# Optimization experiments

Hardware: AMD Instinct MI355X
Metric: run time of the kernel (lower is better)

Reference implementation:

```python
import jax, jax.numpy as jnp
import numpy as np

GROUPS = 8
HEADS = 8
EPS = 1e-5


def group_norm(x, w, b, groups=GROUPS, eps=EPS):
    # x: [B, C, D, H, W]
    B, C, D, H, W = x.shape
    xg = x.reshape(B, groups, C // groups, D, H, W)
    mu = xg.mean(axis=(2, 3, 4, 5), keepdims=True)
    var = xg.var(axis=(2, 3, 4, 5), keepdims=True)
    xn = ((xg - mu) / jnp.sqrt(var + eps)).reshape(B, C, D, H, W)
    return xn * w[None, :, None, None, None] + b[None, :, None, None, None]


def conv1x1(x, w, b):
    # 1x1x1 Conv3d == channel-mixing GEMM. w: [Cout, Cin], x: [B, Cin, D, H, W]
    y = jnp.einsum('oc,bcdhw->bodhw', w, x)
    return y + b[None, :, None, None, None]


def setup_inputs() -> dict:
    key = jax.random.key(0)
    ks = jax.random.split(key, 8)
    C, CTX = 512, 512
    B, D, H, W = 1, 16, 16, 16
    x = jax.random.normal(ks[0], (B, C, D, H, W), dtype=jnp.float32)
    context = jax.random.normal(ks[1], (B, CTX, D, H, W), dtype=jnp.float32)
    return {
        'x': x,
        'context': context,
        'norm_w': jnp.ones((C,), jnp.float32),
        'norm_b': jnp.zeros((C,), jnp.float32),
        'normc_w': jnp.ones((CTX,), jnp.float32),
        'normc_b': jnp.zeros((CTX,), jnp.float32),
        'q_w': jax.random.normal(ks[2], (C, C), jnp.float32) * 0.02,
        'q_b': jnp.zeros((C,), jnp.float32),
        'kv_w': jax.random.normal(ks[3], (2 * C, CTX), jnp.float32) * 0.02,
        'kv_b': jnp.zeros((2 * C,), jnp.float32),
        'proj_w': jax.random.normal(ks[4], (C, C), jnp.float32) * 0.02,
        'proj_b': jnp.zeros((C,), jnp.float32),
    }


def _split_heads(t, heads):
    # [B, (h c), D, H, W] -> [B, h, S, c] with S = D*H*W
    B, C, D, H, W = t.shape
    return t.reshape(B, heads, C // heads, D * H * W).transpose(0, 1, 3, 2)


def reference(x, context, norm_w, norm_b, normc_w, normc_b,
              q_w, q_b, kv_w, kv_b, proj_w, proj_b):
    B, C, D, H, W = x.shape
    h = group_norm(x, norm_w, norm_b)
    c = group_norm(context, normc_w, normc_b)
    q = conv1x1(h, q_w, q_b)
    kv = conv1x1(c, kv_w, kv_b)
    k, v = jnp.split(kv, 2, axis=1)
    q = _split_heads(q, HEADS)   # [B, h, S, c]
    k = _split_heads(k, HEADS)
    v = _split_heads(v, HEADS)
    scale = (C // HEADS) ** (-0.5)
    logits = jnp.einsum('bhqc,bhkc->bhqk', q, k) * scale
    attn = jax.nn.softmax(logits, axis=-1)
    out = jnp.einsum('bhqk,bhkc->bhqc', attn, v)
    # [B, h, S, c] -> [B, (h c), D, H, W]
    out = out.transpose(0, 1, 3, 2).reshape(B, C, D, H, W)
    out = conv1x1(out, proj_w, proj_b)
    return x + out
```

## Files before the change

### kernel.cpp

```cpp
#include <hip/hip_runtime.h>

typedef unsigned short u16;
typedef unsigned int u32;
typedef float f32x4 __attribute__((ext_vector_type(4)));
typedef __bf16 bf16x8 __attribute__((ext_vector_type(8)));
typedef u32 u32x4 __attribute__((ext_vector_type(4)));
typedef u32 u32x2 __attribute__((ext_vector_type(2)));
typedef short s16x4 __attribute__((ext_vector_type(4)));

#define LOG2E 1.44269504088896340736f

static __device__ __forceinline__ u16 f2bf(float f){ u32 u=__builtin_bit_cast(u32,f); u32 r=u+0x7fffu+((u>>16)&1u); return (u16)(r>>16); }
static __device__ __forceinline__ u32 pk2(float a,float b){ return (u32)f2bf(a)|((u32)f2bf(b)<<16); }
static __device__ __forceinline__ float fexp2(float x){
#if __has_builtin(__builtin_amdgcn_exp2f)
  return __builtin_amdgcn_exp2f(x);
#else
  float r; asm volatile("v_exp_f32 %0, %1" : "=v"(r) : "v"(x)); return r;
#endif
}
static __device__ __forceinline__ f32x4 mfma16(u32x4 a,u32x4 b,f32x4 c){
  return __builtin_amdgcn_mfma_f32_16x16x32_bf16(__builtin_bit_cast(bf16x8,a),__builtin_bit_cast(bf16x8,b),c,0,0,0);
}
#if __has_builtin(__builtin_amdgcn_mfma_f32_16x16x16bf16_1k)
static __device__ __forceinline__ f32x4 mfma1k(s16x4 a,s16x4 b,f32x4 c){
  return __builtin_amdgcn_mfma_f32_16x16x16bf16_1k(a,b,c,0,0,0);
}
#else
static __device__ __forceinline__ f32x4 mfma1k(s16x4 a,s16x4 b,f32x4 c){
  f32x4 d; asm("v_mfma_f32_16x16x16_bf16 %0, %1, %2, %3":"=v"(d):"v"(a),"v"(b),"v"(c)); return d;
}
#endif
static __device__ __forceinline__ u32x4 ldfrag(const u32* p){
  uint2 a=*(const uint2*)p; uint2 b=*(const uint2*)(p+2);
  u32x4 r; r.x=a.x; r.y=a.y; r.z=b.x; r.w=b.y; return r;
}
static __device__ __forceinline__ s16x4 ld8(const u32* p){
  return __builtin_bit_cast(s16x4, *(const u32x2*)p);
}
static __device__ __forceinline__ void stlds(u32* d, uint4 v){
  *(uint2*)d = make_uint2(v.x,v.y); *(uint2*)(d+2) = make_uint2(v.z,v.w);
}
static __device__ __forceinline__ uint4 pack8(float4 a,float4 b){
  uint4 o; o.x=pk2(a.x,a.y); o.y=pk2(a.z,a.w); o.z=pk2(b.x,b.y); o.w=pk2(b.z,b.w); return o;
}

__global__ __launch_bounds__(256) void k_stats(const float* __restrict__ x, const float* __restrict__ c,
                                               float* __restrict__ stats){
  const int g=blockIdx.x>>3, slice=blockIdx.x&7;
  const float* src=(g<8?x:c)+(size_t)(g&7)*262144+(size_t)slice*32768;
  const float4* p=(const float4*)src;
  const int t=threadIdx.x;
  float s1=0.f,s2=0.f;
  for(int i=0;i<32;i++){
    float4 v=p[t+i*256];
    s1+=v.x+v.y+v.z+v.w;
    s2+=v.x*v.x+v.y*v.y+v.z*v.z+v.w*v.w;
  }
  #pragma unroll
  for(int m=1;m<64;m<<=1){ s1+=__shfl_xor(s1,m,64); s2+=__shfl_xor(s2,m,64); }
  __shared__ float r1[4],r2[4];
  const int lane=t&63,w=t>>6;
  if(lane==0){ r1[w]=s1; r2[w]=s2; }
  __syncthreads();
  if(t==0){
    atomicAdd(&stats[2*g],   r1[0]+r1[1]+r1[2]+r1[3]);
    atomicAdd(&stats[2*g+1], r2[0]+r2[1]+r2[2]+r2[3]);
  }
}

__global__ __launch_bounds__(256) void k_prep(const float* __restrict__ qw,const float* __restrict__ qb,
    const float* __restrict__ kvw,const float* __restrict__ kvb,
    const float* __restrict__ nw,const float* __restrict__ nb,
    const float* __restrict__ ncw,const float* __restrict__ ncb,
    const float* __restrict__ pb,const float* __restrict__ stats,
    u16* __restrict__ Wall,float* __restrict__ biasAll){
  const int lane=threadIdx.x&63, w=threadIdx.x>>6;
  const int r=blockIdx.x*4+w;
  if(r>=1536){ if(lane==0) biasAll[r]=pb[r-1536]; return; }
  const bool isq = r<512;
  const float* Wsrc = isq ? qw+(size_t)r*512 : kvw+(size_t)(r-512)*512;
  const float* anw = isq ? nw : ncw;
  const float* anb = isq ? nb : ncb;
  const int gbase = isq ? 0 : 8;
  const float bin = isq ? qb[r] : kvb[r-512];
  const int ci0=lane*8;
  float4 wa=*(const float4*)(Wsrc+ci0);
  float4 wb=*(const float4*)(Wsrc+ci0+4);
  float wf[8]={wa.x,wa.y,wa.z,wa.w,wb.x,wb.y,wb.z,wb.w};
  float bp=0.f; u16 hb[8];
  #pragma unroll
  for(int j=0;j<8;j++){
    int ci=ci0+j;
    int g=gbase+(ci>>6);
    float mean=stats[2*g]*(1.f/262144.f);
    float var =stats[2*g+1]*(1.f/262144.f)-mean*mean;
    float rstd=rsqrtf(var+1e-5f);
    float alv=anw[ci]*rstd;
    float bev=anb[ci]-mean*alv;
    bp+=wf[j]*bev;
    hb[j]=f2bf(wf[j]*alv);
  }
  uint4 ov;
  ov.x=(u32)hb[0]|((u32)hb[1]<<16);
  ov.y=(u32)hb[2]|((u32)hb[3]<<16);
  ov.z=(u32)hb[4]|((u32)hb[5]<<16);
  ov.w=(u32)hb[6]|((u32)hb[7]<<16);
  *(uint4*)(Wall+(size_t)r*512+ci0)=ov;
  #pragma unroll
  for(int m=1;m<64;m<<=1) bp+=__shfl_xor(bp,m,64);
  if(lane==0) biasAll[r]=bin+bp;
}

template<int AMODE,int BMODE,int SMODE,int ZM>
__global__ __launch_bounds__(256) void k_gemm(const void* __restrict__ Av,const void* __restrict__ Av2,
    const void* __restrict__ Bv,const float* __restrict__ biasAll,const float* __restrict__ residf,
    void* __restrict__ out1,void* __restrict__ out2,float scale1,float scale2){
  __shared__ __align__(16) u32 As[2][64*18];
  __shared__ __align__(16) u32 Bs[2][128*18];
  const int t=threadIdx.x, lane=t&63, w=t>>6;
  const int wm=w&1, wn=w>>1, quad=lane>>4, l15=lane&15;
  const int m0=blockIdx.y*64, n0=blockIdx.x*128;
  const int z = ZM ? blockIdx.z : 0;
  const void* Aptr = (ZM && z) ? Av2 : Av;
  const u16* Bu = (const u16*)Bv + (BMODE==0 ? (size_t)z*512*512 : 0);
  const float* Bf = (const float*)Bv;
  const float* bias = biasAll + (ZM ? z*512 : 0);
  void* outv = (ZM && z) ? out2 : out1;
  const float scale = (ZM && z) ? scale2 : scale1;
  const int arow=t>>2, akc=(t&3)*8;
  const int cl=t>>3, s8=(t&7)*8;

  uint4 ra; float4 raf0, raf1;
  uint4 rb0, rb1; float4 rbf0, rbf1, rbf2, rbf3;

  auto loadAB=[&](int kk){
    if(AMODE==0){
      const u16* A=(const u16*)Aptr;
      ra=*(const uint4*)(A+(size_t)(m0+arow)*512+kk+akc);
    }else if(AMODE==1){
      const float* A=(const float*)Aptr;
      raf0=*(const float4*)(A+(size_t)(kk+cl)*4096+m0+s8);
      raf1=*(const float4*)(A+(size_t)(kk+cl)*4096+m0+s8+4);
    }else{
      const float* A=(const float*)Aptr;
      raf0=*(const float4*)(A+(size_t)(m0+arow)*512+kk+akc);
      raf1=*(const float4*)(A+(size_t)(m0+arow)*512+kk+akc+4);
    }
    if(BMODE==2){
      rbf0=*(const float4*)(Bf+(size_t)(kk+cl)*4096+n0+s8);
      rbf1=*(const float4*)(Bf+(size_t)(kk+cl)*4096+n0+s8+4);
      rbf2=*(const float4*)(Bf+(size_t)(kk+cl)*4096+n0+64+s8);
      rbf3=*(const float4*)(Bf+(size_t)(kk+cl)*4096+n0+64+s8+4);
    }else if(BMODE==1){
      rb0=*(const uint4*)(Bu+((size_t)((kk>>6)*4096+n0+arow))*64+(kk&63)+akc);
      rb1=*(const uint4*)(Bu+((size_t)((kk>>6)*4096+n0+64+arow))*64+(kk&63)+akc);
    }else{
      rb0=*(const uint4*)(Bu+(size_t)(n0+arow)*512+kk+akc);
      rb1=*(const uint4*)(Bu+(size_t)(n0+64+arow)*512+kk+akc);
    }
  };
  auto writeAB=[&](u32* Asb,u32* Bsb){
    if(AMODE==0){ stlds(&Asb[arow*18+(akc>>1)],ra); }
    else if(AMODE==1){
      float f[8]={raf0.x,raf0.y,raf0.z,raf0.w,raf1.x,raf1.y,raf1.z,raf1.w};
      u16* As16=(u16*)Asb;
      #pragma unroll
      for(int j=0;j<8;j++) As16[(s8+j)*36+cl]=f2bf(f[j]);
    }else{
      stlds(&Asb[arow*18+(akc>>1)],pack8(raf0,raf1));
    }
    if(BMODE==2){
      u16* Bs16=(u16*)Bsb;
      float f[8]={rbf0.x,rbf0.y,rbf0.z,rbf0.w,rbf1.x,rbf1.y,rbf1.z,rbf1.w};
      float g[8]={rbf2.x,rbf2.y,rbf2.z,rbf2.w,rbf3.x,rbf3.y,rbf3.z,rbf3.w};
      #pragma unroll
      for(int j=0;j<8;j++){
        Bs16[(s8+j)*36+cl]=f2bf(f[j]);
        Bs16[(64+s8+j)*36+cl]=f2bf(g[j]);
      }
    }else{
      stlds(&Bsb[arow*18+(akc>>1)],rb0);
      stlds(&Bsb[(64+arow)*18+(akc>>1)],rb1);
    }
  };

  f32x4 acc[2][4];
  #pragma unroll
  for(int i=0;i<2;i++)
    #pragma unroll
    for(int j=0;j<4;j++){ acc[i][j].x=0.f; acc[i][j].y=0.f; acc[i][j].z=0.f; acc[i][j].w=0.f; }

  auto compute=[&](const u32* Asb,const u32* Bsb){
    const u32* Ab=Asb+(wm*32+l15)*18+quad*4;
    const u32* Bb=Bsb+(wn*64+l15)*18+quad*4;
    u32x4 af[2], bfr[4];
    #pragma unroll
    for(int mt=0;mt<2;mt++) af[mt]=ldfrag(Ab+mt*288);
    #pragma unroll
    for(int nt=0;nt<4;nt++) bfr[nt]=ldfrag(Bb+nt*288);
    #pragma unroll
    for(int mt=0;mt<2;mt++)
      #pragma unroll
      for(int nt=0;nt<4;nt++) acc[mt][nt]=mfma16(af[mt],bfr[nt],acc[mt][nt]);
  };

  loadAB(0); writeAB(As[0],Bs[0]);
  __syncthreads();
  for(int kk=0;kk<512;kk+=64){
    loadAB(kk+32);
    compute(As[0],Bs[0]);
    writeAB(As[1],Bs[1]);
    __syncthreads();
    const bool n2=(kk+64)<512;
    if(n2) loadAB(kk+64);
    compute(As[1],Bs[1]);
    if(n2){ writeAB(As[0],Bs[0]); __syncthreads(); }
  }
  #pragma unroll
  for(int mt=0;mt<2;mt++)
    #pragma unroll
    for(int nt=0;nt<4;nt++){
      const int n = n0 + wn*64 + nt*16 + l15;
      if(SMODE==0){
        u16* out=(u16*)outv;
        const float bn = bias[n];
        const size_t base = ((size_t)((n>>6)*4096))*64 + (size_t)(n&63);
        #pragma unroll
        for(int r=0;r<4;r++){
          int m = m0 + wm*32 + mt*16 + quad*4 + r;
          out[base + (size_t)m*64] = f2bf((acc[mt][nt][r]+bn)*scale);
        }
      } else if(SMODE==1){
        u16* out=(u16*)outv;
        #pragma unroll
        for(int r=0;r<4;r++){
          int m = m0 + wm*32 + mt*16 + quad*4 + r;
          out[(size_t)m*4096+n] = f2bf(acc[mt][nt][r] + bias[m]);
        }
      } else {
        float* out=(float*)outv;
        #pragma unroll
        for(int r=0;r<4;r++){
          int m = m0 + wm*32 + mt*16 + quad*4 + r;
          out[(size_t)m*4096+n] = acc[mt][nt][r] + bias[m] + residf[(size_t)m*4096+n];
        }
      }
    }
}

__global__ __launch_bounds__(512,4) void k_attn(const u16* __restrict__ Qh,const u16* __restrict__ Kh,
                                              const u16* __restrict__ Vp,u16* __restrict__ Oh){
  __shared__ __align__(16) u32 KS[2][2][64*34];
  __shared__ __align__(16) u32 VS[2][2][64*34];
  const int t=threadIdx.x, lane=t&63, w=t>>6, quad=lane>>4, l15=lane&15;
  const int half=w>>2, wq=w&3;
  const int h=blockIdx.y, s0=blockIdx.x*64;
  const int tt=t&255, srow=tt>>2, sc=(tt&3)*16;
  const u16* Kg = Kh + ((size_t)(h*4096 + half*2048 + srow))*64 + sc;
  const u16* Vg = Vp + (size_t)(h*64+srow)*4096 + half*2048 + sc;
  const u16* Qg = Qh + ((size_t)(h*4096+s0+wq*16+l15))*64;
  s16x4 qf[4];
  #pragma unroll
  for(int kc=0;kc<4;kc++) qf[kc]=ld8((const u32*)(Qg + kc*16 + quad*4));

  uint4 pk0,pk1,pv0,pv1;
  auto loadKV=[&](int t0l){
    const u16* kp=Kg+(size_t)t0l*64;
    pk0=*(const uint4*)kp; pk1=*(const uint4*)(kp+8);
    const u16* vp=Vg+t0l;
    pv0=*(const uint4*)vp; pv1=*(const uint4*)(vp+8);
  };
  auto writeKV=[&](u32* Kb,u32* Vb){
    u32* kw=Kb+srow*34+(sc>>1);
    stlds(kw,pk0); stlds(kw+4,pk1);
    u32* vw=Vb+srow*34+(sc>>1);
    stlds(vw,pv0); stlds(vw+4,pv1);
  };

  float lrun=0.f; f32x4 oacc[4];
  #pragma unroll
  for(int cn=0;cn<4;cn++){ oacc[cn].x=0.f; oacc[cn].y=0.f; oacc[cn].z=0.f; oacc[cn].w=0.f; }

  auto tilestep=[&](const u32* Kb,const u32* Vb){
    f32x4 sv[4];
    #pragma unroll
    for(int nt=0;nt<4;nt++){
      const u32* kb=Kb+(nt*16+l15)*34+quad*2;
      f32x4 a; a.x=0.f; a.y=0.f; a.z=0.f; a.w=0.f;
      #pragma unroll
      for(int kc=0;kc<4;kc++) a=mfma1k(ld8(kb+kc*8),qf[kc],a);
      sv[nt]=a;
    }
    s16x4 pfr[4];
    #pragma unroll
    for(int nt=0;nt<4;nt++){
      float p0=fexp2(sv[nt].x),p1=fexp2(sv[nt].y),p2=fexp2(sv[nt].z),p3=fexp2(sv[nt].w);
      lrun+=(p0+p1)+(p2+p3);
      u32x2 pp;
      pp.x=(__builtin_bit_cast(u32,p0)>>16)|(__builtin_bit_cast(u32,p1)&0xffff0000u);
      pp.y=(__builtin_bit_cast(u32,p2)>>16)|(__builtin_bit_cast(u32,p3)&0xffff0000u);
      pfr[nt]=__builtin_bit_cast(s16x4,pp);
    }
    #pragma unroll
    for(int cn=0;cn<4;cn++){
      const u32* vb=Vb+(cn*16+l15)*34+quad*2;
      f32x4 a=oacc[cn];
      #pragma unroll
      for(int nt=0;nt<4;nt++) a=mfma1k(pfr[nt],ld8(vb+nt*8),a);
      oacc[cn]=a;
    }
  };

  loadKV(0); writeKV(KS[half][0],VS[half][0]);
  __syncthreads();
  for(int t0=0;t0<2048;t0+=128){
    loadKV(t0+64);
    tilestep(KS[half][0],VS[half][0]);
    writeKV(KS[half][1],VS[half][1]);
    __syncthreads();
    const bool more=(t0+128)<2048;
    if(more) loadKV(t0+128);
    tilestep(KS[half][1],VS[half][1]);
    if(more){ writeKV(KS[half][0],VS[half][0]); __syncthreads(); }
  }
  __syncthreads();
  float* cb=(float*)KS[1];
  const int cbi=(wq*64+lane)*17;
  if(half==1){
    #pragma unroll
    for(int cn=0;cn<4;cn++)
      #pragma unroll
      for(int r=0;r<4;r++) cb[cbi+cn*4+r]=oacc[cn][r];
    cb[cbi+16]=lrun;
  }
  __syncthreads();
  if(half==0){
    #pragma unroll
    for(int cn=0;cn<4;cn++)
      #pragma unroll
      for(int r=0;r<4;r++) oacc[cn][r]+=cb[cbi+cn*4+r];
    lrun+=cb[cbi+16];
    float l=lrun;
    l+=__shfl_xor(l,16,64);
    l+=__shfl_xor(l,32,64);
    #pragma unroll
    for(int r=0;r<4;r++){
      float inv=1.f/__shfl(l,quad*4+r,64);
      #pragma unroll
      for(int cn=0;cn<4;cn++)
        Oh[((size_t)(h*4096+s0+wq*16+quad*4+r))*64 + cn*16 + l15]=f2bf(oacc[cn][r]*inv);
    }
  }
}

extern "C" void kernel_launch(void* const* d_in, const int* in_sizes, int n_in,
                              void* d_out, int out_size, void* d_ws, size_t ws_size,
                              hipStream_t stream){
  (void)in_sizes; (void)n_in; (void)out_size; (void)ws_size;
  const float* x  =(const float*)d_in[0];
  const float* ctx=(const float*)d_in[1];
  const float* nw =(const float*)d_in[2];
  const float* nb =(const float*)d_in[3];
  const float* ncw=(const float*)d_in[4];
  const float* ncb=(const float*)d_in[5];
  const float* qw =(const float*)d_in[6];
  const float* qb =(const float*)d_in[7];
  const float* kvw=(const float*)d_in[8];
  const float* kvb=(const float*)d_in[9];
  const float* pw =(const float*)d_in[10];
  const float* pb =(const float*)d_in[11];
  float* out=(float*)d_out;
  char* ws=(char*)d_ws;
  float* stats  =(float*)ws;
  float* biasAll=(float*)(ws+256);
  u16* Wall=(u16*)(ws+16384);
  u16* Qh  =(u16*)(ws+1589248);
  u16* Kh  =(u16*)(ws+5783552);
  u16* Vp  =(u16*)(ws+9977856);
  u16* Oh  =(u16*)(ws+14172160);

  (void)hipMemsetAsync(stats,0,128,stream);
  k_stats<<<dim3(128),dim3(256),0,stream>>>(x,ctx,stats);
  k_prep<<<dim3(512),dim3(256),0,stream>>>(qw,qb,kvw,kvb,nw,nb,ncw,ncb,pb,stats,Wall,biasAll);
  k_gemm<1,0,0,1><<<dim3(4,64,2),dim3(256),0,stream>>>(x, ctx, Wall, biasAll, nullptr, Qh, Kh, 0.125f*LOG2E, 1.f);
  k_gemm<0,2,1,0><<<dim3(32,8),dim3(256),0,stream>>>(Wall+(size_t)1024*512, nullptr, ctx, biasAll+1024, nullptr, Vp, nullptr, 1.f, 1.f);
  k_attn<<<dim3(64,8),dim3(512),0,stream>>>(Qh,Kh,Vp,Oh);
  k_gemm<2,1,2,0><<<dim3(32,8),dim3(256),0,stream>>>(pw, nullptr, Oh, biasAll+1536, x, out, nullptr, 1.f, 1.f);
}
```

Before: 189.7 us.

## Fuse group-norm into QKV GEMM, merge Q/K/V launches, drop weight prep kernel

Removes the weight-folding prep kernel and the stats memset. k_stats now writes per-block partial sums without atomics, and a single QKV kernel reduces them, applies the group-norm affine to activations while loading them into shared memory, and converts the weights to bf16 on the fly. The separate Q/K and V GEMM launches are merged into one 768-block grid. The attention QK^T step switches from the 16x16x16 MFMA to the 16x16x32 MFMA with wider fragment loads. This trades launch count and the Wall weight round-trip through memory for extra per-element FMA and fp32 weight reads inside every GEMM tile, and changes rounding because normalization is now applied to activations rather than folded into the weights.

```diff
diff --git a/kernel.cpp b/kernel.cpp
--- a/kernel.cpp
+++ b/kernel.cpp
@@ -64,124 +64,94 @@
   if(lane==0){ r1[w]=s1; r2[w]=s2; }
   __syncthreads();
   if(t==0){
-    atomicAdd(&stats[2*g],   r1[0]+r1[1]+r1[2]+r1[3]);
-    atomicAdd(&stats[2*g+1], r2[0]+r2[1]+r2[2]+r2[3]);
-  }
-}
-
-__global__ __launch_bounds__(256) void k_prep(const float* __restrict__ qw,const float* __restrict__ qb,
+    stats[blockIdx.x*2  ]=r1[0]+r1[1]+r1[2]+r1[3];
+    stats[blockIdx.x*2+1]=r2[0]+r2[1]+r2[2]+r2[3];
+  }
+}
+
+__global__ __launch_bounds__(256) void k_qkv(const float* __restrict__ x,const float* __restrict__ ctx,
+    const float* __restrict__ qw,const float* __restrict__ qb,
     const float* __restrict__ kvw,const float* __restrict__ kvb,
     const float* __restrict__ nw,const float* __restrict__ nb,
     const float* __restrict__ ncw,const float* __restrict__ ncb,
-    const float* __restrict__ pb,const float* __restrict__ stats,
-    u16* __restrict__ Wall,float* __restrict__ biasAll){
-  const int lane=threadIdx.x&63, w=threadIdx.x>>6;
-  const int r=blockIdx.x*4+w;
-  if(r>=1536){ if(lane==0) biasAll[r]=pb[r-1536]; return; }
-  const bool isq = r<512;
-  const float* Wsrc = isq ? qw+(size_t)r*512 : kvw+(size_t)(r-512)*512;
-  const float* anw = isq ? nw : ncw;
-  const float* anb = isq ? nb : ncb;
-  const int gbase = isq ? 0 : 8;
-  const float bin = isq ? qb[r] : kvb[r-512];
-  const int ci0=lane*8;
-  float4 wa=*(const float4*)(Wsrc+ci0);
-  float4 wb=*(const float4*)(Wsrc+ci0+4);
-  float wf[8]={wa.x,wa.y,wa.z,wa.w,wb.x,wb.y,wb.z,wb.w};
-  float bp=0.f; u16 hb[8];
-  #pragma unroll
-  for(int j=0;j<8;j++){
-    int ci=ci0+j;
-    int g=gbase+(ci>>6);
-    float mean=stats[2*g]*(1.f/262144.f);
-    float var =stats[2*g+1]*(1.f/262144.f)-mean*mean;
-    float rstd=rsqrtf(var+1e-5f);
-    float alv=anw[ci]*rstd;
-    float bev=anb[ci]-mean*alv;
-    bp+=wf[j]*bev;
-    hb[j]=f2bf(wf[j]*alv);
-  }
-  uint4 ov;
-  ov.x=(u32)hb[0]|((u32)hb[1]<<16);
-  ov.y=(u32)hb[2]|((u32)hb[3]<<16);
-  ov.z=(u32)hb[4]|((u32)hb[5]<<16);
-  ov.w=(u32)hb[6]|((u32)hb[7]<<16);
-  *(uint4*)(Wall+(size_t)r*512+ci0)=ov;
-  #pragma unroll
-  for(int m=1;m<64;m<<=1) bp+=__shfl_xor(bp,m,64);
-  if(lane==0) biasAll[r]=bin+bp;
-}
-
-template<int AMODE,int BMODE,int SMODE,int ZM>
-__global__ __launch_bounds__(256) void k_gemm(const void* __restrict__ Av,const void* __restrict__ Av2,
-    const void* __restrict__ Bv,const float* __restrict__ biasAll,const float* __restrict__ residf,
-    void* __restrict__ out1,void* __restrict__ out2,float scale1,float scale2){
+    const float* __restrict__ stats,
+    u16* __restrict__ Qh,u16* __restrict__ Kh,u16* __restrict__ Vp,float qscale){
   __shared__ __align__(16) u32 As[2][64*18];
   __shared__ __align__(16) u32 Bs[2][128*18];
-  const int t=threadIdx.x, lane=t&63, w=t>>6;
+  __shared__ float AB[1024];
+  __shared__ float mr[16];
+  const int bid=blockIdx.x, t=threadIdx.x, lane=t&63, w=t>>6;
   const int wm=w&1, wn=w>>1, quad=lane>>4, l15=lane&15;
-  const int m0=blockIdx.y*64, n0=blockIdx.x*128;
-  const int z = ZM ? blockIdx.z : 0;
-  const void* Aptr = (ZM && z) ? Av2 : Av;
-  const u16* Bu = (const u16*)Bv + (BMODE==0 ? (size_t)z*512*512 : 0);
-  const float* Bf = (const float*)Bv;
-  const float* bias = biasAll + (ZM ? z*512 : 0);
-  void* outv = (ZM && z) ? out2 : out1;
-  const float scale = (ZM && z) ? scale2 : scale1;
+  const bool isV = bid>=512;
+  const int z = isV ? 1 : (bid>>8);
+  int m0,n0;
+  if(isV){ int v=bid-512; n0=(v&31)*128; m0=(v>>5)*64; }
+  else   { int r=bid&255; n0=(r&3)*128; m0=(r>>2)*64; }
+  const float* anw = z ? ncw : nw;
+  const float* anb = z ? ncb : nb;
+  if(t<8){
+    const int gb = z ? 8 : 0;
+    float s1=0.f,s2=0.f;
+    #pragma unroll
+    for(int s=0;s<8;s++){ s1+=stats[((gb+t)*8+s)*2]; s2+=stats[((gb+t)*8+s)*2+1]; }
+    float mean=s1*(1.f/262144.f);
+    float var =s2*(1.f/262144.f)-mean*mean;
+    mr[t*2]=mean; mr[t*2+1]=rsqrtf(var+1e-5f);
+  }
+  __syncthreads();
+  #pragma unroll
+  for(int i=0;i<2;i++){
+    int ci=t+i*256, g=ci>>6;
+    float al=anw[ci]*mr[g*2+1];
+    AB[ci]=al; AB[512+ci]=anb[ci]-mr[g*2]*al;
+  }
+  __syncthreads();
+
   const int arow=t>>2, akc=(t&3)*8;
   const int cl=t>>3, s8=(t&7)*8;
-
-  uint4 ra; float4 raf0, raf1;
-  uint4 rb0, rb1; float4 rbf0, rbf1, rbf2, rbf3;
+  const float* act = z ? ctx : x;
+  const float* W   = z ? kvw : qw;
+  float4 ta0,ta1,tb0,tb1,tb2,tb3;
+  int kpend=0;
 
   auto loadAB=[&](int kk){
-    if(AMODE==0){
-      const u16* A=(const u16*)Aptr;
-      ra=*(const uint4*)(A+(size_t)(m0+arow)*512+kk+akc);
-    }else if(AMODE==1){
-      const float* A=(const float*)Aptr;
-      raf0=*(const float4*)(A+(size_t)(kk+cl)*4096+m0+s8);
-      raf1=*(const float4*)(A+(size_t)(kk+cl)*4096+m0+s8+4);
+    kpend=kk;
+    if(!isV){
+      ta0=*(const float4*)(act+(size_t)(kk+cl)*4096+m0+s8);
+      ta1=*(const float4*)(act+(size_t)(kk+cl)*4096+m0+s8+4);
+      tb0=*(const float4*)(W+(size_t)(n0+arow)*512+kk+akc);
+      tb1=*(const float4*)(W+(size_t)(n0+arow)*512+kk+akc+4);
+      tb2=*(const float4*)(W+(size_t)(n0+64+arow)*512+kk+akc);
+      tb3=*(const float4*)(W+(size_t)(n0+64+arow)*512+kk+akc+4);
     }else{
-      const float* A=(const float*)Aptr;
-      raf0=*(const float4*)(A+(size_t)(m0+arow)*512+kk+akc);
-      raf1=*(const float4*)(A+(size_t)(m0+arow)*512+kk+akc+4);
-    }
-    if(BMODE==2){
-      rbf0=*(const float4*)(Bf+(size_t)(kk+cl)*4096+n0+s8);
-      rbf1=*(const float4*)(Bf+(size_t)(kk+cl)*4096+n0+s8+4);
-      rbf2=*(const float4*)(Bf+(size_t)(kk+cl)*4096+n0+64+s8);
-      rbf3=*(const float4*)(Bf+(size_t)(kk+cl)*4096+n0+64+s8+4);
-    }else if(BMODE==1){
-      rb0=*(const uint4*)(Bu+((size_t)((kk>>6)*4096+n0+arow))*64+(kk&63)+akc);
-      rb1=*(const uint4*)(Bu+((size_t)((kk>>6)*4096+n0+64+arow))*64+(kk&63)+akc);
+      ta0=*(const float4*)(kvw+(size_t)(512+m0+arow)*512+kk+akc);
+      ta1=*(const float4*)(kvw+(size_t)(512+m0+arow)*512+kk+akc+4);
+      tb0=*(const float4*)(ctx+(size_t)(kk+cl)*4096+n0+s8);
+      tb1=*(const float4*)(ctx+(size_t)(kk+cl)*4096+n0+s8+4);
+      tb2=*(const float4*)(ctx+(size_t)(kk+cl)*4096+n0+64+s8);
+      tb3=*(const float4*)(ctx+(size_t)(kk+cl)*4096+n0+64+s8+4);
+    }
+  };
+  auto writeAB=[&](u32* Asb,u32* Bsb){
+    if(!isV){
+      const float al=AB[kpend+cl], bt=AB[512+kpend+cl];
+      float f[8]={ta0.x,ta0.y,ta0.z,ta0.w,ta1.x,ta1.y,ta1.z,ta1.w};
+      u16* As16=(u16*)Asb;
+      #pragma unroll
+      for(int j=0;j<8;j++) As16[(s8+j)*36+cl]=f2bf(al*f[j]+bt);
+      stlds(&Bsb[arow*18+(akc>>1)],pack8(tb0,tb1));
+      stlds(&Bsb[(64+arow)*18+(akc>>1)],pack8(tb2,tb3));
     }else{
-      rb0=*(const uint4*)(Bu+(size_t)(n0+arow)*512+kk+akc);
-      rb1=*(const uint4*)(Bu+(size_t)(n0+64+arow)*512+kk+akc);
-    }
-  };
-  auto writeAB=[&](u32* Asb,u32* Bsb){
-    if(AMODE==0){ stlds(&Asb[arow*18+(akc>>1)],ra); }
-    else if(AMODE==1){
-      float f[8]={raf0.x,raf0.y,raf0.z,raf0.w,raf1.x,raf1.y,raf1.z,raf1.w};
-      u16* As16=(u16*)Asb;
-      #pragma unroll
-      for(int j=0;j<8;j++) As16[(s8+j)*36+cl]=f2bf(f[j]);
-    }else{
-      stlds(&Asb[arow*18+(akc>>1)],pack8(raf0,raf1));
-    }
-    if(BMODE==2){
+      stlds(&Asb[arow*18+(akc>>1)],pack8(ta0,ta1));
+      const float al=AB[kpend+cl], bt=AB[512+kpend+cl];
+      float f[8]={tb0.x,tb0.y,tb0.z,tb0.w,tb1.x,tb1.y,tb1.z,tb1.w};
+      float g[8]={tb2.x,tb2.y,tb2.z,tb2.w,tb3.x,tb3.y,tb3.z,tb3.w};
       u16* Bs16=(u16*)Bsb;
-      float f[8]={rbf0.x,rbf0.y,rbf0.z,rbf0.w,rbf1.x,rbf1.y,rbf1.z,rbf1.w};
-      float g[8]={rbf2.x,rbf2.y,rbf2.z,rbf2.w,rbf3.x,rbf3.y,rbf3.z,rbf3.w};
       #pragma unroll
       for(int j=0;j<8;j++){
-        Bs16[(s8+j)*36+cl]=f2bf(f[j]);
-        Bs16[(64+s8+j)*36+cl]=f2bf(g[j]);
+        Bs16[(s8+j)*36+cl]=f2bf(al*f[j]+bt);
+        Bs16[(64+s8+j)*36+cl]=f2bf(al*g[j]+bt);
       }
-    }else{
-      stlds(&Bsb[arow*18+(akc>>1)],rb0);
-      stlds(&Bsb[(64+arow)*18+(akc>>1)],rb1);
     }
   };
 
@@ -222,29 +192,85 @@
     #pragma unroll
     for(int nt=0;nt<4;nt++){
       const int n = n0 + wn*64 + nt*16 + l15;
-      if(SMODE==0){
-        u16* out=(u16*)outv;
-        const float bn = bias[n];
+      if(!isV){
+        u16* out = z ? Kh : Qh;
+        const float scale = z ? 1.f : qscale;
+        const float bn = (z ? kvb[n] : qb[n]);
         const size_t base = ((size_t)((n>>6)*4096))*64 + (size_t)(n&63);
         #pragma unroll
         for(int r=0;r<4;r++){
           int m = m0 + wm*32 + mt*16 + quad*4 + r;
           out[base + (size_t)m*64] = f2bf((acc[mt][nt][r]+bn)*scale);
         }
-      } else if(SMODE==1){
-        u16* out=(u16*)outv;
+      } else {
         #pragma unroll
         for(int r=0;r<4;r++){
           int m = m0 + wm*32 + mt*16 + quad*4 + r;
-          out[(size_t)m*4096+n] = f2bf(acc[mt][nt][r] + bias[m]);
+          Vp[(size_t)m*4096+n] = f2bf(acc[mt][nt][r] + kvb[512+m]);
         }
-      } else {
-        float* out=(float*)outv;
-        #pragma unroll
-        for(int r=0;r<4;r++){
-          int m = m0 + wm*32 + mt*16 + quad*4 + r;
-          out[(size_t)m*4096+n] = acc[mt][nt][r] + bias[m] + residf[(size_t)m*4096+n];
-        }
+      }
+    }
+}
+
+__global__ __launch_bounds__(256) void k_proj(const float* __restrict__ A,const u16* __restrict__ B,
+    const float* __restrict__ bias,const float* __restrict__ residf,float* __restrict__ out){
+  __shared__ __align__(16) u32 As[2][64*18];
+  __shared__ __align__(16) u32 Bs[2][128*18];
+  const int t=threadIdx.x, lane=t&63, w=t>>6;
+  const int wm=w&1, wn=w>>1, quad=lane>>4, l15=lane&15;
+  const int m0=blockIdx.y*64, n0=blockIdx.x*128;
+  const int arow=t>>2, akc=(t&3)*8;
+  float4 ra0,ra1; uint4 rb0,rb1;
+  auto loadAB=[&](int kk){
+    ra0=*(const float4*)(A+(size_t)(m0+arow)*512+kk+akc);
+    ra1=*(const float4*)(A+(size_t)(m0+arow)*512+kk+akc+4);
+    rb0=*(const uint4*)(B+((size_t)((kk>>6)*4096+n0+arow))*64+(kk&63)+akc);
+    rb1=*(const uint4*)(B+((size_t)((kk>>6)*4096+n0+64+arow))*64+(kk&63)+akc);
+  };
+  auto writeAB=[&](u32* Asb,u32* Bsb){
+    stlds(&Asb[arow*18+(akc>>1)],pack8(ra0,ra1));
+    stlds(&Bsb[arow*18+(akc>>1)],rb0);
+    stlds(&Bsb[(64+arow)*18+(akc>>1)],rb1);
+  };
+  f32x4 acc[2][4];
+  #pragma unroll
+  for(int i=0;i<2;i++)
+    #pragma unroll
+    for(int j=0;j<4;j++){ acc[i][j].x=0.f; acc[i][j].y=0.f; acc[i][j].z=0.f; acc[i][j].w=0.f; }
+  auto compute=[&](const u32* Asb,const u32* Bsb){
+    const u32* Ab=Asb+(wm*32+l15)*18+quad*4;
+    const u32* Bb=Bsb+(wn*64+l15)*18+quad*4;
+    u32x4 af[2], bfr[4];
+    #pragma unroll
+    for(int mt=0;mt<2;mt++) af[mt]=ldfrag(Ab+mt*288);
+    #pragma unroll
+    for(int nt=0;nt<4;nt++) bfr[nt]=ldfrag(Bb+nt*288);
+    #pragma unroll
+    for(int mt=0;mt<2;mt++)
+      #pragma unroll
+      for(int nt=0;nt<4;nt++) acc[mt][nt]=mfma16(af[mt],bfr[nt],acc[mt][nt]);
+  };
+  loadAB(0); writeAB(As[0],Bs[0]);
+  __syncthreads();
+  for(int kk=0;kk<512;kk+=64){
+    loadAB(kk+32);
+    compute(As[0],Bs[0]);
+    writeAB(As[1],Bs[1]);
+    __syncthreads();
+    const bool n2=(kk+64)<512;
+    if(n2) loadAB(kk+64);
+    compute(As[1],Bs[1]);
+    if(n2){ writeAB(As[0],Bs[0]); __syncthreads(); }
+  }
+  #pragma unroll
+  for(int mt=0;mt<2;mt++)
+    #pragma unroll
+    for(int nt=0;nt<4;nt++){
+      const int n = n0 + wn*64 + nt*16 + l15;
+      #pragma unroll
+      for(int r=0;r<4;r++){
+        int m = m0 + wm*32 + mt*16 + quad*4 + r;
+        out[(size_t)m*4096+n] = acc[mt][nt][r] + bias[m] + residf[(size_t)m*4096+n];
       }
     }
 }
@@ -259,10 +285,10 @@
   const int tt=t&255, srow=tt>>2, sc=(tt&3)*16;
   const u16* Kg = Kh + ((size_t)(h*4096 + half*2048 + srow))*64 + sc;
   const u16* Vg = Vp + (size_t)(h*64+srow)*4096 + half*2048 + sc;
-  const u16* Qg = Qh + ((size_t)(h*4096+s0+wq*16+l15))*64;
-  s16x4 qf[4];
-  #pragma unroll
-  for(int kc=0;kc<4;kc++) qf[kc]=ld8((const u32*)(Qg + kc*16 + quad*4));
+  const u32* Qg = (const u32*)(Qh + ((size_t)(h*4096+s0+wq*16+l15))*64);
+  u32x4 qfw[2];
+  qfw[0]=ldfrag(Qg + quad*4);
+  qfw[1]=ldfrag(Qg + 16 + quad*4);
 
   uint4 pk0,pk1,pv0,pv1;
   auto loadKV=[&](int t0l){
@@ -286,10 +312,10 @@
     f32x4 sv[4];
     #pragma unroll
     for(int nt=0;nt<4;nt++){
-      const u32* kb=Kb+(nt*16+l15)*34+quad*2;
+      const u32* kb=Kb+(nt*16+l15)*34+quad*4;
       f32x4 a; a.x=0.f; a.y=0.f; a.z=0.f; a.w=0.f;
-      #pragma unroll
-      for(int kc=0;kc<4;kc++) a=mfma1k(ld8(kb+kc*8),qf[kc],a);
+      a=mfma16(ldfrag(kb),qfw[0],a);
+      a=mfma16(ldfrag(kb+16),qfw[1],a);
       sv[nt]=a;
     }
     s16x4 pfr[4];
@@ -372,19 +398,14 @@
   const float* pb =(const float*)d_in[11];
   float* out=(float*)d_out;
   char* ws=(char*)d_ws;
-  float* stats  =(float*)ws;
-  float* biasAll=(float*)(ws+256);
-  u16* Wall=(u16*)(ws+16384);
-  u16* Qh  =(u16*)(ws+1589248);
-  u16* Kh  =(u16*)(ws+5783552);
-  u16* Vp  =(u16*)(ws+9977856);
-  u16* Oh  =(u16*)(ws+14172160);
-
-  (void)hipMemsetAsync(stats,0,128,stream);
+  float* stats=(float*)ws;
+  u16* Qh  =(u16*)(ws+16384);
+  u16* Kh  =(u16*)(ws+16384+4194304);
+  u16* Vp  =(u16*)(ws+16384+2*4194304);
+  u16* Oh  =(u16*)(ws+16384+3*4194304);
+
   k_stats<<<dim3(128),dim3(256),0,stream>>>(x,ctx,stats);
-  k_prep<<<dim3(512),dim3(256),0,stream>>>(qw,qb,kvw,kvb,nw,nb,ncw,ncb,pb,stats,Wall,biasAll);
-  k_gemm<1,0,0,1><<<dim3(4,64,2),dim3(256),0,stream>>>(x, ctx, Wall, biasAll, nullptr, Qh, Kh, 0.125f*LOG2E, 1.f);
-  k_gemm<0,2,1,0><<<dim3(32,8),dim3(256),0,stream>>>(Wall+(size_t)1024*512, nullptr, ctx, biasAll+1024, nullptr, Vp, nullptr, 1.f, 1.f);
+  k_qkv<<<dim3(768),dim3(256),0,stream>>>(x,ctx,qw,qb,kvw,kvb,nw,nb,ncw,ncb,stats,Qh,Kh,Vp,0.125f*LOG2E);
   k_attn<<<dim3(64,8),dim3(512),0,stream>>>(Qh,Kh,Vp,Oh);
-  k_gemm<2,1,2,0><<<dim3(32,8),dim3(256),0,stream>>>(pw, nullptr, Oh, biasAll+1536, x, out, nullptr, 1.f, 1.f);
-}
+  k_proj<<<dim3(32,8),dim3(256),0,stream>>>(pw,Oh,pb,x,out);
+}
```

New measurement: 176.4 us. -7.0%, faster.
